# Performance work log

Hardware: AMD Instinct MI355X
Metric: run time of the kernel (lower is better)

## Reference

```python
import jax, jax.numpy as jnp
import numpy as np

NC = 120000            # active coarse voxels
D, H, W = 16, 256, 256 # coarse grid
NF = 2 * NC            # active fine voxels (upsample output)
CIN, COUT = 128, 64


def _build_pairs():
    """Build spconv-style (in_idx, out_idx) pair maps per kernel offset.
    Padding: in_idx = NC (dummy zero feature row), out_idx = n_out (dropped row)."""
    rng = np.random.default_rng(0)
    flat = rng.choice(D * H * W, size=NC, replace=False)
    cz, cy, cx = np.unravel_index(flat, (D, H, W))
    lut = np.full(D * H * W, -1, np.int64)
    lut[flat] = np.arange(NC)

    def subm(offs):
        P = np.full((len(offs), NC, 2), NC, np.int32)
        for k, (dz, dy, dx) in enumerate(offs):
            nz, ny, nx = cz + dz, cy + dy, cx + dx
            ok = (nz >= 0) & (nz < D) & (ny >= 0) & (ny < H) & (nx >= 0) & (nx < W)
            nb = np.full(NC, -1, np.int64)
            nb[ok] = lut[(nz[ok] * H + ny[ok]) * W + nx[ok]]
            ok &= nb >= 0
            idx = np.nonzero(ok)[0]
            P[k, :len(idx), 0] = nb[idx]
            P[k, :len(idx), 1] = idx
        return P

    o33 = [(a, b, c) for a in (-1, 0, 1) for b in (-1, 0, 1) for c in (-1, 0, 1)]
    o13 = [(0, b, c) for b in (-1, 0, 1) for c in (-1, 0, 1)]   # kernel (1,3,3)
    o31 = [(a, 0, c) for a in (-1, 0, 1) for c in (-1, 0, 1)]   # kernel (3,1,3)

    # fine coords: each coarse voxel c spawns fine voxels 2c and 2c+1 (all dims)
    fz = np.concatenate([cz * 2, cz * 2 + 1])
    fy = np.concatenate([cy * 2, cy * 2 + 1])
    fx = np.concatenate([cx * 2, cx * 2 + 1])
    # inverse of a k=3, stride=2, pad=1 downsample: fine f <- coarse o where f = 2o - 1 + k
    Pu = np.zeros((27, NC, 2), np.int32)
    Pu[..., 0] = NC
    Pu[..., 1] = NF
    for k, (a, b, c) in enumerate([(a, b, c) for a in range(3) for b in range(3) for c in range(3)]):
        nz, ny, nx = fz + 1 - a, fy + 1 - b, fx + 1 - c
        ok = (nz % 2 == 0) & (ny % 2 == 0) & (nx % 2 == 0) & (nz >= 0) & (ny >= 0) & (nx >= 0)
        oz, oy, ox = nz // 2, ny // 2, nx // 2
        ok &= (oz < D) & (oy < H) & (ox < W)
        nb = np.full(NF, -1, np.int64)
        nb[ok] = lut[(oz[ok] * H + oy[ok]) * W + ox[ok]]
        ok &= nb >= 0
        idx = np.nonzero(ok)[0][:NC]
        Pu[k, :len(idx), 0] = nb[idx]
        Pu[k, :len(idx), 1] = idx
    return subm(o33), subm(o13), subm(o31), Pu


def setup_inputs():
    p33, p13, p31, pup = _build_pairs()
    ks = jax.random.split(jax.random.key(0), 12)
    f32 = jnp.float32
    return {
        "feats_x": jax.random.normal(ks[0], (NC, CIN), f32),
        "feats_skip": jax.random.normal(ks[1], (NC, CIN), f32),
        "W_trans": 0.05 * jax.random.normal(ks[2], (27, CIN, COUT), f32),
        "W1": 0.05 * jax.random.normal(ks[3], (9, COUT, COUT), f32),
        "W2": 0.05 * jax.random.normal(ks[4], (9, COUT, COUT), f32),
        "W_up": 0.05 * jax.random.normal(ks[5], (27, COUT, COUT), f32),
        "g0": 1.0 + 0.1 * jax.random.normal(ks[6], (COUT,), f32),
        "b0": 0.1 * jax.random.normal(ks[7], (COUT,), f32),
        "g1": 1.0 + 0.1 * jax.random.normal(ks[8], (COUT,), f32),
        "b1": 0.1 * jax.random.normal(ks[9], (COUT,), f32),
        "g2": 1.0 + 0.1 * jax.random.normal(ks[10], (COUT,), f32),
        "b2": 0.1 * jax.random.normal(ks[11], (COUT,), f32),
        "pairs33": jnp.asarray(p33),
        "pairs13": jnp.asarray(p13),
        "pairs31": jnp.asarray(p31),
        "pairs_up": jnp.asarray(pup),
    }


def _spconv(feats, Wk, pairs, n_out):
    # gather-GEMM-scatter sparse conv: feats [N,Cin], Wk [K,Cin,Cout], pairs [K,P,2]
    fp = jnp.concatenate([feats, jnp.zeros((1, feats.shape[1]), feats.dtype)], 0)
    out = jnp.zeros((n_out + 1, Wk.shape[2]), feats.dtype)
    for k in range(Wk.shape[0]):  # fixed small K (9 or 27)
        msg = fp[pairs[k, :, 0]] @ Wk[k]        # [P, Cout]
        out = out.at[pairs[k, :, 1]].add(msg)
    return out[:n_out]


def _bn(x, g, b):
    # BatchNorm1d (training-mode batch stats, eps=1e-5, biased var)
    m = x.mean(0)
    v = x.var(0)
    return (x - m) * jax.lax.rsqrt(v + 1e-5) * g + b


def reference(feats_x, feats_skip, W_trans, W1, W2, W_up,
              g0, b0, g1, b1, g2, b2,
              pairs33, pairs13, pairs31, pairs_up):
    x = feats_x + feats_skip                              # residual fuse with skip
    upA = _spconv(x, W_trans, pairs33, NC)                # trans_dilao (3x3x3 subm)
    upA = _bn(jax.nn.leaky_relu(upA, 0.01), g0, b0)       # act then BN (as in source)
    upE1 = _bn(_spconv(upA, W1, pairs13, NC), g1, b1)     # conv1x3 + bn1
    upE2 = _bn(_spconv(upA, W2, pairs31, NC), g2, b2)     # conv3x1 + bn2
    return _spconv(upE1 + upE2, W_up, pairs_up, NF)       # SparseInverseConv3d upsample
```

## Files before the change

kernel.cpp:

```cpp
#include <hip/hip_runtime.h>
#include <stdint.h>

typedef unsigned short u16;
typedef unsigned int u32;
typedef __bf16 bf16x8 __attribute__((ext_vector_type(8)));
typedef float floatx4 __attribute__((ext_vector_type(4)));

static constexpr int NC = 120000;
static constexpr int NF = 240000;

__device__ __forceinline__ float bf2f(u16 u) {
    union { u32 i; float f; } v; v.i = ((u32)u) << 16; return v.f;
}
__device__ __forceinline__ u16 f2bf(float f) {
    union { float f; u32 i; } v; v.f = f;
    u32 r = v.i + 0x7FFFu + ((v.i >> 16) & 1u);
    return (u16)(r >> 16);
}

__global__ void add_pad_k(const float* __restrict__ a, const float* __restrict__ b,
                          u16* __restrict__ xp) {
    int idx = blockIdx.x * blockDim.x + threadIdx.x;
    if (idx >= (NC + 1) * 32) return;
    uint2 vo;
    if (idx < NC * 32) {
        float4 va = ((const float4*)a)[idx];
        float4 vb = ((const float4*)b)[idx];
        vo.x = (u32)f2bf(va.x + vb.x) | ((u32)f2bf(va.y + vb.y) << 16);
        vo.y = (u32)f2bf(va.z + vb.z) | ((u32)f2bf(va.w + vb.w) << 16);
    } else {
        vo.x = vo.y = 0u;
    }
    ((uint2*)xp)[idx] = vo;
}

__global__ void transpose_w_k(const float* __restrict__ W, u16* __restrict__ Wt,
                              int K, int Cin) {
    int idx = blockIdx.x * blockDim.x + threadIdx.x;
    if (idx >= K * Cin * 64) return;
    int per = Cin * 64;
    int k = idx / per, rem = idx - k * per;
    int kc = rem >> 11;
    int r2 = rem & 2047;
    int nt = r2 >> 9, lane = (r2 >> 3) & 63, j = r2 & 7;
    int ci = kc * 32 + (lane >> 4) * 8 + j;
    int co = nt * 16 + (lane & 15);
    Wt[idx] = f2bf(W[(size_t)(k * Cin + ci) * 64 + co]);
}

__device__ __forceinline__ int upslot_to_k(int s) {
    if (s == 4) return 13;
    int e = s < 4 ? s : s - 5;
    int base = s < 4 ? 0 : 18;
    return base + 2 * e + ((e >> 1) << 1);
}
__global__ void transpose_wup_k(const float* __restrict__ W, u16* __restrict__ Wt) {
    int idx = blockIdx.x * blockDim.x + threadIdx.x;
    if (idx >= 9 * 4096) return;
    int s = idx >> 12, rem = idx & 4095;
    int kc = rem >> 11, r2 = rem & 2047;
    int nt = r2 >> 9, lane = (r2 >> 3) & 63, j = r2 & 7;
    int ci = kc * 32 + (lane >> 4) * 8 + j;
    int co = nt * 16 + (lane & 15);
    int k = upslot_to_k(s);
    Wt[idx] = f2bf(W[(size_t)(k * 64 + ci) * 64 + co]);
}

__global__ void fill_k(int* __restrict__ p, int n, int val) {
    int i = blockIdx.x * blockDim.x + threadIdx.x;
    if (i < n) p[i] = val;
}

__global__ void scatter_k(const int* __restrict__ pairs, int* __restrict__ inv,
                          int npairs, int n_out) {
    int i = blockIdx.x * blockDim.x + threadIdx.x;
    if (i >= npairs) return;
    int in = pairs[2 * i], out = pairs[2 * i + 1];
    if (out < n_out) inv[(i / NC) * n_out + out] = in;
}

__global__ void scatter_up_k(const int* __restrict__ pairs, int* __restrict__ inv) {
    int i = blockIdx.x * blockDim.x + threadIdx.x;
    if (i >= 27 * NC) return;
    int in = pairs[2 * i], out = pairs[2 * i + 1];
    if (out >= NF) return;
    int k = i / NC;
    int a = k / 9, r = k - a * 9, b = r / 3, c = r - b * 3;
    int s;
    if (k == 13) {
        s = 4;
    } else if (((a | b | c) & 1) == 0) {
        int e = (a >> 1) * 4 + (b >> 1) * 2 + (c >> 1);
        s = e < 4 ? e : e + 1;
    } else {
        return;
    }
    inv[(size_t)s * NF + out] = in;
}

template <int TCIN, int K, int R, bool LEAKY, bool F32OUT, int MINW>
__global__ __launch_bounds__(256, MINW) void spconv_k(
    const u16* __restrict__ feats,
    const int* __restrict__ invA, const u16* __restrict__ wTA, void* __restrict__ outA,
    const int* __restrict__ invB, const u16* __restrict__ wTB, void* __restrict__ outB,
    int nb0, int n_outA, int n_outB) {
    constexpr int KC = TCIN / 32;
    const int tid = threadIdx.x;
    const int wave = tid >> 6, lane = tid & 63;
    const int l15 = lane & 15, quad = lane >> 4;
    const bool second = (int)blockIdx.x >= nb0;
    const int bid = second ? (int)blockIdx.x - nb0 : (int)blockIdx.x;
    const int* __restrict__ inv = second ? invB : invA;
    const u16* __restrict__ wT  = second ? wTB : wTA;
    void* __restrict__ outv     = second ? outB : outA;
    const int n_out             = second ? n_outB : n_outA;

    const int blockrow = bid * (R * 64);
    const int base = blockrow + wave * 16 + l15;

    floatx4 acc[R][4];
#pragma unroll
    for (int t = 0; t < R; ++t)
#pragma unroll
        for (int nt = 0; nt < 4; ++nt) acc[t][nt] = (floatx4)(0.0f);

    int rc[R], rn[R];
#pragma unroll
    for (int t = 0; t < R; ++t) rc[t] = inv[base + t * 64];
#pragma unroll
    for (int t = 0; t < R; ++t) rn[t] = inv[n_out + base + t * 64];

    bf16x8 abuf[2][R][KC];
#pragma unroll
    for (int t = 0; t < R; ++t) {
        if (__any(rc[t] != NC)) {
            const u16* ap = feats + (size_t)rc[t] * TCIN + quad * 8;
#pragma unroll
            for (int kc = 0; kc < KC; ++kc) abuf[0][t][kc] = *(const bf16x8*)(ap + kc * 32);
        }
    }

#pragma unroll
    for (int k = 0; k < K; ++k) {
        const int cur = k & 1, nxt = cur ^ 1;
        int rf[R];
#pragma unroll
        for (int t = 0; t < R; ++t) rf[t] = NC;
        if (k + 2 < K) {
            const int* invf = inv + (size_t)(k + 2) * n_out;
#pragma unroll
            for (int t = 0; t < R; ++t) rf[t] = invf[base + t * 64];
        }
        bool lv[R], any = false;
#pragma unroll
        for (int t = 0; t < R; ++t) { lv[t] = __any(rc[t] != NC); any = any || lv[t]; }
        bf16x8 b[KC][4];
        if (any) {
            const u16* wk = wT + (size_t)k * (64 * TCIN);
#pragma unroll
            for (int kc = 0; kc < KC; ++kc)
#pragma unroll
                for (int nt = 0; nt < 4; ++nt)
                    b[kc][nt] = *(const bf16x8*)(wk + ((kc * 4 + nt) * 64 + lane) * 8);
        }
        if (k + 1 < K) {
#pragma unroll
            for (int t = 0; t < R; ++t) {
                if (__any(rn[t] != NC)) {
                    const u16* ap = feats + (size_t)rn[t] * TCIN + quad * 8;
#pragma unroll
                    for (int kc = 0; kc < KC; ++kc) abuf[nxt][t][kc] = *(const bf16x8*)(ap + kc * 32);
                }
            }
        }
#pragma unroll
        for (int t = 0; t < R; ++t) {
            if (lv[t]) {
#pragma unroll
                for (int kc = 0; kc < KC; ++kc)
#pragma unroll
                    for (int nt = 0; nt < 4; ++nt)
                        acc[t][nt] = __builtin_amdgcn_mfma_f32_16x16x32_bf16(
                            abuf[cur][t][kc], b[kc][nt], acc[t][nt], 0, 0, 0);
            }
        }
#pragma unroll
        for (int t = 0; t < R; ++t) { rc[t] = rn[t]; rn[t] = rf[t]; }
    }
#pragma unroll
    for (int t = 0; t < R; ++t) {
#pragma unroll
        for (int nt = 0; nt < 4; ++nt) {
#pragma unroll
            for (int r = 0; r < 4; ++r) {
                float v = acc[t][nt][r];
                if (LEAKY) v = v > 0.f ? v : 0.01f * v;
                int row = blockrow + t * 64 + wave * 16 + quad * 4 + r;
                size_t oi = (size_t)row * 64 + nt * 16 + l15;
                if (F32OUT) ((float*)outv)[oi] = v;
                else        ((u16*)outv)[oi] = f2bf(v);
            }
        }
    }
}

__global__ void stats2_k(const u16* __restrict__ ra, const u16* __restrict__ rb,
                         float* __restrict__ sa, float* __restrict__ sb, int half) {
    const u16* raw = ((int)blockIdx.x < half) ? ra : rb;
    float* sums    = ((int)blockIdx.x < half) ? sa : sb;
    int bx = ((int)blockIdx.x < half) ? (int)blockIdx.x : (int)blockIdx.x - half;
    int tid = threadIdx.x;
    int wave = tid >> 6, c = tid & 63;
    int gw = bx * 4 + wave;
    int GW = half * 4;
    float s = 0.f, q = 0.f;
    for (int r = gw; r < NC; r += GW) {
        float v = bf2f(raw[(size_t)r * 64 + c]);
        s += v; q += v * v;
    }
    __shared__ float sbm[4][64], qbm[4][64];
    sbm[wave][c] = s; qbm[wave][c] = q;
    __syncthreads();
    if (tid < 64) {
        float S = sbm[0][tid] + sbm[1][tid] + sbm[2][tid] + sbm[3][tid];
        float Q = qbm[0][tid] + qbm[1][tid] + qbm[2][tid] + qbm[3][tid];
        atomicAdd(&sums[tid], S);
        atomicAdd(&sums[64 + tid], Q);
    }
}

template <bool F32IN>
__global__ void stats_pair_k(const void* __restrict__ ra, const void* __restrict__ rb,
                             float* __restrict__ sums, int nblk) {
    int tid = threadIdx.x;
    int wave = tid >> 6, c = tid & 63;
    int gw = (int)blockIdx.x * 4 + wave;
    int GW = nblk * 4;
    float s = 0.f, q = 0.f;
    for (int r = gw; r < NC; r += GW) {
        size_t o = (size_t)r * 64 + c;
        float v = F32IN ? (((const float*)ra)[o] + ((const float*)rb)[o])
                        : (bf2f(((const u16*)ra)[o]) + bf2f(((const u16*)rb)[o]));
        v = v > 0.f ? v : 0.01f * v;
        s += v; q += v * v;
    }
    __shared__ float sbm[4][64], qbm[4][64];
    sbm[wave][c] = s; qbm[wave][c] = q;
    __syncthreads();
    if (tid < 64) {
        float S = sbm[0][tid] + sbm[1][tid] + sbm[2][tid] + sbm[3][tid];
        float Q = qbm[0][tid] + qbm[1][tid] + qbm[2][tid] + qbm[3][tid];
        atomicAdd(&sums[tid], S);
        atomicAdd(&sums[64 + tid], Q);
    }
}

__global__ void finalize_k(const float* __restrict__ sums, const float* __restrict__ g,
                           const float* __restrict__ bb, float* __restrict__ scsh) {
    int c = threadIdx.x;
    if (c < 64) {
        float m = sums[c] / (float)NC;
        float v = sums[64 + c] / (float)NC - m * m;
        float sc = g[c] * rsqrtf(v + 1e-5f);
        scsh[c] = sc;
        scsh[64 + c] = bb[c] - m * sc;
    }
}

template <bool F32IN>
__global__ void apply_pair_k(const void* __restrict__ ra, const void* __restrict__ rb,
                             const float* __restrict__ scsh, u16* __restrict__ up) {
    int idx = blockIdx.x * blockDim.x + threadIdx.x;
    if (idx >= (NC + 1) * 64) return;
    int c = idx & 63, i = idx >> 6;
    u16 o = 0;
    if (i < NC) {
        float v = F32IN ? (((const float*)ra)[idx] + ((const float*)rb)[idx])
                        : (bf2f(((const u16*)ra)[idx]) + bf2f(((const u16*)rb)[idx]));
        v = v > 0.f ? v : 0.01f * v;
        o = f2bf(v * scsh[c] + scsh[64 + c]);
    }
    up[idx] = o;
}

__global__ void apply12_k(const u16* __restrict__ rb, const u16* __restrict__ rc,
                          const float* __restrict__ s1, const float* __restrict__ s2,
                          u16* __restrict__ up) {
    int idx = blockIdx.x * blockDim.x + threadIdx.x;
    if (idx >= (NC + 1) * 64) return;
    int c = idx & 63, i = idx >> 6;
    float v = bf2f(rb[idx]) * s1[c] + s1[64 + c] + bf2f(rc[idx]) * s2[c] + s2[64 + c];
    up[idx] = (i < NC) ? f2bf(v) : (u16)0;
}

extern "C" void kernel_launch(void* const* d_in, const int* in_sizes, int n_in,
                              void* d_out, int out_size, void* d_ws, size_t ws_size,
                              hipStream_t stream) {
    const float* feats_x    = (const float*)d_in[0];
    const float* feats_skip = (const float*)d_in[1];
    const float* W_trans    = (const float*)d_in[2];
    const float* W1         = (const float*)d_in[3];
    const float* W2         = (const float*)d_in[4];
    const float* W_up       = (const float*)d_in[5];
    const float* g0 = (const float*)d_in[6],  *b0 = (const float*)d_in[7];
    const float* g1 = (const float*)d_in[8],  *b1 = (const float*)d_in[9];
    const float* g2 = (const float*)d_in[10], *b2 = (const float*)d_in[11];
    const int* pairs33 = (const int*)d_in[12];
    const int* pairs13 = (const int*)d_in[13];
    const int* pairs31 = (const int*)d_in[14];
    const int* pairs_up = (const int*)d_in[15];
    float* outp = (float*)d_out;

    const bool bigws = ws_size >= (size_t)130267392;

    char* ws = (char*)d_ws;
    size_t off = 0;
    auto alloc = [&](size_t bytes) {
        char* p = ws + off;
        off += (bytes + 255) & ~(size_t)255;
        return p;
    };
    u16* xp    = (u16*)alloc(30720256);
    int* inv33 = (int*)alloc(13440000);
    int* inv13 = (int*)alloc(4320000);
    int* inv31 = (int*)alloc(4320000);
    void* rawF0 = (void*)alloc(bigws ? 30720000 : 15360000);
    void* rawF1 = (void*)alloc(bigws ? 30720000 : 15360000);
    u16* upA   = (u16*)alloc(15360128);
    u16* WtA   = (u16*)alloc(27 * 128 * 64 * 2);
    u16* Wt1   = (u16*)alloc(9 * 64 * 64 * 2);
    u16* Wt2   = (u16*)alloc(9 * 64 * 64 * 2);
    u16* WtU   = (u16*)alloc(9 * 64 * 64 * 2);
    float* stats = (float*)alloc(6 * 128 * 4);
    int* inv_up = (int*)xp;
    u16* rawB = (u16*)rawF0;
    u16* rawC = (u16*)rawF1;
    u16* upE  = (u16*)inv33;
    float *sums0 = stats,        *sums1 = stats + 128, *sums2 = stats + 256;
    float *scsh0 = stats + 384,  *scsh1 = stats + 512, *scsh2 = stats + 640;

    const int B = 256;
    hipMemsetAsync(stats, 0, 6 * 128 * 4, stream);

    transpose_w_k<<<(27 * 128 * 64 + 255) / 256, B, 0, stream>>>(W_trans, WtA, 27, 128);
    transpose_w_k<<<(9 * 64 * 64 + 255) / 256, B, 0, stream>>>(W1, Wt1, 9, 64);
    transpose_w_k<<<(9 * 64 * 64 + 255) / 256, B, 0, stream>>>(W2, Wt2, 9, 64);
    transpose_wup_k<<<(9 * 64 * 64 + 255) / 256, B, 0, stream>>>(W_up, WtU);

    add_pad_k<<<((NC + 1) * 32 + 255) / 256, B, 0, stream>>>(feats_x, feats_skip, xp);

    fill_k<<<(46 * NC + 255) / 256, B, 0, stream>>>(inv33, 46 * NC, NC);
    scatter_k<<<(27 * NC + 255) / 256, B, 0, stream>>>(pairs33, inv33, 27 * NC, NC);
    scatter_k<<<(9 * NC + 255) / 256, B, 0, stream>>>(pairs13, inv13, 9 * NC, NC);
    scatter_k<<<(9 * NC + 255) / 256, B, 0, stream>>>(pairs31, inv31, 9 * NC, NC);

    if (bigws) {
        spconv_k<128, 14, 3, false, true, 2><<<1250, B, 0, stream>>>(
            xp, inv33, WtA, rawF0, inv33 + 14 * NC, WtA + 14 * 128 * 64, rawF1,
            625, NC, NC);
        stats_pair_k<true><<<240, B, 0, stream>>>(rawF0, rawF1, sums0, 240);
        finalize_k<<<1, 64, 0, stream>>>(sums0, g0, b0, scsh0);
        apply_pair_k<true><<<((NC + 1) * 64 + 255) / 256, B, 0, stream>>>(
            rawF0, rawF1, scsh0, upA);
    } else {
        spconv_k<128, 14, 3, false, false, 2><<<1250, B, 0, stream>>>(
            xp, inv33, WtA, rawF0, inv33 + 14 * NC, WtA + 14 * 128 * 64, rawF1,
            625, NC, NC);
        stats_pair_k<false><<<240, B, 0, stream>>>(rawF0, rawF1, sums0, 240);
        finalize_k<<<1, 64, 0, stream>>>(sums0, g0, b0, scsh0);
        apply_pair_k<false><<<((NC + 1) * 64 + 255) / 256, B, 0, stream>>>(
            rawF0, rawF1, scsh0, upA);
    }

    fill_k<<<(9 * NF + 255) / 256, B, 0, stream>>>(inv_up, 9 * NF, NC);
    scatter_up_k<<<(27 * NC + 255) / 256, B, 0, stream>>>(pairs_up, inv_up);

    spconv_k<64, 9, 3, false, false, 3><<<1250, B, 0, stream>>>(
        upA, inv13, Wt1, rawB, inv31, Wt2, rawC, 625, NC, NC);
    stats2_k<<<240, B, 0, stream>>>(rawB, rawC, sums1, sums2, 120);
    finalize_k<<<1, 64, 0, stream>>>(sums1, g1, b1, scsh1);
    finalize_k<<<1, 64, 0, stream>>>(sums2, g2, b2, scsh2);

    apply12_k<<<((NC + 1) * 64 + 255) / 256, B, 0, stream>>>(rawB, rawC, scsh1, scsh2, upE);

    spconv_k<64, 9, 3, false, true, 3><<<1250, B, 0, stream>>>(
        upE, inv_up, WtU, outp, inv_up, WtU, outp, 1250, NF, NF);
}
```

Measured before the change: 540.7 us.

## Stage weights through LDS and skip provably empty upsample kernel offsets

Each block now copies its per-offset weight slice from global memory into a double-buffered LDS array and reads it from there, with a block barrier after every offset. The first conv uses a runtime live-offset count (14 and 13) instead of running a padded 28th slice, so the inv33 buffer shrinks by one slice. The upsample slots are reordered so the centre offset comes first. The upsample conv is then split: rows below NC run only the centre offset, and rows at or above NC run only the eight corner offsets. This removes weight fetches that every wave repeated and skips offsets known to have no pairs, at the cost of extra barriers and LDS use that may lower occupancy.

```diff
diff --git a/kernel.cpp b/kernel.cpp
--- a/kernel.cpp
+++ b/kernel.cpp
@@ -49,10 +49,9 @@
 }
 
 __device__ __forceinline__ int upslot_to_k(int s) {
-    if (s == 4) return 13;
-    int e = s < 4 ? s : s - 5;
-    int base = s < 4 ? 0 : 18;
-    return base + 2 * e + ((e >> 1) << 1);
+    if (s == 0) return 13;
+    int e = s - 1;
+    return 18 * ((e >> 2) & 1) + 6 * ((e >> 1) & 1) + 2 * (e & 1);
 }
 __global__ void transpose_wup_k(const float* __restrict__ W, u16* __restrict__ Wt) {
     int idx = blockIdx.x * blockDim.x + threadIdx.x;
@@ -88,23 +87,26 @@
     int a = k / 9, r = k - a * 9, b = r / 3, c = r - b * 3;
     int s;
     if (k == 13) {
-        s = 4;
+        s = 0;
     } else if (((a | b | c) & 1) == 0) {
-        int e = (a >> 1) * 4 + (b >> 1) * 2 + (c >> 1);
-        s = e < 4 ? e : e + 1;
+        s = 1 + (a >> 1) * 4 + (b >> 1) * 2 + (c >> 1);
     } else {
         return;
     }
     inv[(size_t)s * NF + out] = in;
 }
 
-template <int TCIN, int K, int R, bool LEAKY, bool F32OUT, int MINW>
+template <int TCIN, int KMAX, int R, bool F32OUT, int MINW>
 __global__ __launch_bounds__(256, MINW) void spconv_k(
     const u16* __restrict__ feats,
     const int* __restrict__ invA, const u16* __restrict__ wTA, void* __restrict__ outA,
     const int* __restrict__ invB, const u16* __restrict__ wTB, void* __restrict__ outB,
-    int nb0, int n_outA, int n_outB) {
+    int nb0, int n_outA, int n_outB, int kliveA, int kliveB) {
     constexpr int KC = TCIN / 32;
+    constexpr int WFRAGS = TCIN * 64 / 8;
+    constexpr int NST = WFRAGS / 256;
+    __shared__ bf16x8 wlds[2][WFRAGS];
+
     const int tid = threadIdx.x;
     const int wave = tid >> 6, lane = tid & 63;
     const int l15 = lane & 15, quad = lane >> 4;
@@ -114,6 +116,7 @@
     const u16* __restrict__ wT  = second ? wTB : wTA;
     void* __restrict__ outv     = second ? outB : outA;
     const int n_out             = second ? n_outB : n_outA;
+    const int Klive             = second ? kliveB : kliveA;
 
     const int blockrow = bid * (R * 64);
     const int base = blockrow + wave * 16 + l15;
@@ -129,6 +132,12 @@
     for (int t = 0; t < R; ++t) rc[t] = inv[base + t * 64];
 #pragma unroll
     for (int t = 0; t < R; ++t) rn[t] = inv[n_out + base + t * 64];
+
+    {
+        const bf16x8* wsrc = (const bf16x8*)wT + tid;
+#pragma unroll
+        for (int s = 0; s < NST; ++s) wlds[0][tid + s * 256] = wsrc[s * 256];
+    }
 
     bf16x8 abuf[2][R][KC];
 #pragma unroll
@@ -139,53 +148,65 @@
             for (int kc = 0; kc < KC; ++kc) abuf[0][t][kc] = *(const bf16x8*)(ap + kc * 32);
         }
     }
-
-#pragma unroll
-    for (int k = 0; k < K; ++k) {
-        const int cur = k & 1, nxt = cur ^ 1;
-        int rf[R];
-#pragma unroll
-        for (int t = 0; t < R; ++t) rf[t] = NC;
-        if (k + 2 < K) {
-            const int* invf = inv + (size_t)(k + 2) * n_out;
-#pragma unroll
-            for (int t = 0; t < R; ++t) rf[t] = invf[base + t * 64];
-        }
-        bool lv[R], any = false;
-#pragma unroll
-        for (int t = 0; t < R; ++t) { lv[t] = __any(rc[t] != NC); any = any || lv[t]; }
-        bf16x8 b[KC][4];
-        if (any) {
-            const u16* wk = wT + (size_t)k * (64 * TCIN);
-#pragma unroll
-            for (int kc = 0; kc < KC; ++kc)
-#pragma unroll
-                for (int nt = 0; nt < 4; ++nt)
-                    b[kc][nt] = *(const bf16x8*)(wk + ((kc * 4 + nt) * 64 + lane) * 8);
-        }
-        if (k + 1 < K) {
-#pragma unroll
-            for (int t = 0; t < R; ++t) {
-                if (__any(rn[t] != NC)) {
-                    const u16* ap = feats + (size_t)rn[t] * TCIN + quad * 8;
-#pragma unroll
-                    for (int kc = 0; kc < KC; ++kc) abuf[nxt][t][kc] = *(const bf16x8*)(ap + kc * 32);
+    __syncthreads();
+
+#pragma unroll
+    for (int k = 0; k < KMAX; ++k) {
+        if (k < Klive) {
+            const int cur = k & 1, nxt = cur ^ 1;
+            if (k + 1 < Klive) {
+                const bf16x8* wsrc = (const bf16x8*)(wT + (size_t)(k + 1) * (64 * TCIN)) + tid;
+                bf16x8 st[NST];
+#pragma unroll
+                for (int s = 0; s < NST; ++s) st[s] = wsrc[s * 256];
+#pragma unroll
+                for (int s = 0; s < NST; ++s) wlds[nxt][tid + s * 256] = st[s];
+            }
+            int rf[R];
+#pragma unroll
+            for (int t = 0; t < R; ++t) rf[t] = NC;
+            if (k + 2 < Klive) {
+                const int* invf = inv + (size_t)(k + 2) * n_out;
+#pragma unroll
+                for (int t = 0; t < R; ++t) rf[t] = invf[base + t * 64];
+            }
+            bool lv[R], any = false;
+#pragma unroll
+            for (int t = 0; t < R; ++t) { lv[t] = __any(rc[t] != NC); any = any || lv[t]; }
+            if (k + 1 < Klive) {
+#pragma unroll
+                for (int t = 0; t < R; ++t) {
+                    if (__any(rn[t] != NC)) {
+                        const u16* ap = feats + (size_t)rn[t] * TCIN + quad * 8;
+#pragma unroll
+                        for (int kc = 0; kc < KC; ++kc)
+                            abuf[nxt][t][kc] = *(const bf16x8*)(ap + kc * 32);
+                    }
                 }
             }
+            if (any) {
+                bf16x8 b[KC][4];
+#pragma unroll
+                for (int kc = 0; kc < KC; ++kc)
+#pragma unroll
+                    for (int nt = 0; nt < 4; ++nt)
+                        b[kc][nt] = wlds[cur][(kc * 4 + nt) * 64 + lane];
+#pragma unroll
+                for (int t = 0; t < R; ++t) {
+                    if (lv[t]) {
+#pragma unroll
+                        for (int kc = 0; kc < KC; ++kc)
+#pragma unroll
+                            for (int nt = 0; nt < 4; ++nt)
+                                acc[t][nt] = __builtin_amdgcn_mfma_f32_16x16x32_bf16(
+                                    abuf[cur][t][kc], b[kc][nt], acc[t][nt], 0, 0, 0);
+                    }
+                }
+            }
+            __syncthreads();
+#pragma unroll
+            for (int t = 0; t < R; ++t) { rc[t] = rn[t]; rn[t] = rf[t]; }
         }
-#pragma unroll
-        for (int t = 0; t < R; ++t) {
-            if (lv[t]) {
-#pragma unroll
-                for (int kc = 0; kc < KC; ++kc)
-#pragma unroll
-                    for (int nt = 0; nt < 4; ++nt)
-                        acc[t][nt] = __builtin_amdgcn_mfma_f32_16x16x32_bf16(
-                            abuf[cur][t][kc], b[kc][nt], acc[t][nt], 0, 0, 0);
-            }
-        }
-#pragma unroll
-        for (int t = 0; t < R; ++t) { rc[t] = rn[t]; rn[t] = rf[t]; }
     }
 #pragma unroll
     for (int t = 0; t < R; ++t) {
@@ -194,7 +215,6 @@
 #pragma unroll
             for (int r = 0; r < 4; ++r) {
                 float v = acc[t][nt][r];
-                if (LEAKY) v = v > 0.f ? v : 0.01f * v;
                 int row = blockrow + t * 64 + wave * 16 + quad * 4 + r;
                 size_t oi = (size_t)row * 64 + nt * 16 + l15;
                 if (F32OUT) ((float*)outv)[oi] = v;
@@ -321,7 +341,7 @@
         return p;
     };
     u16* xp    = (u16*)alloc(30720256);
-    int* inv33 = (int*)alloc(13440000);
+    int* inv33 = (int*)alloc(12960000);
     int* inv13 = (int*)alloc(4320000);
     int* inv31 = (int*)alloc(4320000);
     void* rawF0 = (void*)alloc(bigws ? 30720000 : 15360000);
@@ -349,23 +369,23 @@
 
     add_pad_k<<<((NC + 1) * 32 + 255) / 256, B, 0, stream>>>(feats_x, feats_skip, xp);
 
-    fill_k<<<(46 * NC + 255) / 256, B, 0, stream>>>(inv33, 46 * NC, NC);
+    fill_k<<<(45 * NC + 255) / 256, B, 0, stream>>>(inv33, 45 * NC, NC);
     scatter_k<<<(27 * NC + 255) / 256, B, 0, stream>>>(pairs33, inv33, 27 * NC, NC);
     scatter_k<<<(9 * NC + 255) / 256, B, 0, stream>>>(pairs13, inv13, 9 * NC, NC);
     scatter_k<<<(9 * NC + 255) / 256, B, 0, stream>>>(pairs31, inv31, 9 * NC, NC);
 
     if (bigws) {
-        spconv_k<128, 14, 3, false, true, 2><<<1250, B, 0, stream>>>(
+        spconv_k<128, 14, 3, true, 2><<<1250, B, 0, stream>>>(
             xp, inv33, WtA, rawF0, inv33 + 14 * NC, WtA + 14 * 128 * 64, rawF1,
-            625, NC, NC);
+            625, NC, NC, 14, 13);
         stats_pair_k<true><<<240, B, 0, stream>>>(rawF0, rawF1, sums0, 240);
         finalize_k<<<1, 64, 0, stream>>>(sums0, g0, b0, scsh0);
         apply_pair_k<true><<<((NC + 1) * 64 + 255) / 256, B, 0, stream>>>(
             rawF0, rawF1, scsh0, upA);
     } else {
-        spconv_k<128, 14, 3, false, false, 2><<<1250, B, 0, stream>>>(
+        spconv_k<128, 14, 3, false, 2><<<1250, B, 0, stream>>>(
             xp, inv33, WtA, rawF0, inv33 + 14 * NC, WtA + 14 * 128 * 64, rawF1,
-            625, NC, NC);
+            625, NC, NC, 14, 13);
         stats_pair_k<false><<<240, B, 0, stream>>>(rawF0, rawF1, sums0, 240);
         finalize_k<<<1, 64, 0, stream>>>(sums0, g0, b0, scsh0);
         apply_pair_k<false><<<((NC + 1) * 64 + 255) / 256, B, 0, stream>>>(
@@ -375,14 +395,16 @@
     fill_k<<<(9 * NF + 255) / 256, B, 0, stream>>>(inv_up, 9 * NF, NC);
     scatter_up_k<<<(27 * NC + 255) / 256, B, 0, stream>>>(pairs_up, inv_up);
 
-    spconv_k<64, 9, 3, false, false, 3><<<1250, B, 0, stream>>>(
-        upA, inv13, Wt1, rawB, inv31, Wt2, rawC, 625, NC, NC);
+    spconv_k<64, 9, 3, false, 3><<<1250, B, 0, stream>>>(
+        upA, inv13, Wt1, rawB, inv31, Wt2, rawC, 625, NC, NC, 9, 9);
     stats2_k<<<240, B, 0, stream>>>(rawB, rawC, sums1, sums2, 120);
     finalize_k<<<1, 64, 0, stream>>>(sums1, g1, b1, scsh1);
     finalize_k<<<1, 64, 0, stream>>>(sums2, g2, b2, scsh2);
 
     apply12_k<<<((NC + 1) * 64 + 255) / 256, B, 0, stream>>>(rawB, rawC, scsh1, scsh2, upE);
 
-    spconv_k<64, 9, 3, false, true, 3><<<1250, B, 0, stream>>>(
-        upE, inv_up, WtU, outp, inv_up, WtU, outp, 1250, NF, NF);
-}
+    spconv_k<64, 8, 3, true, 3><<<1250, B, 0, stream>>>(
+        upE, inv_up, WtU, outp,
+        inv_up + (size_t)NF + NC, WtU + 64 * 64, (void*)(outp + (size_t)NC * 64),
+        625, NF, NF, 1, 8);
+}
```

Result: no change. 533.3 us (-1.4%).

## Replace gather-based inverse maps with dense center tap plus atomic scatter over compacted pairs

Applied to the files above, without the earlier changes.

Drops the fill/scatter inverse-map construction. The identity centre tap of each convolution, and the two identity-like upsample taps, are now computed as dense GEMMs that write fp32 outputs directly. The remaining taps are processed over the valid prefix of each pair list, found by binary search, using weights staged in LDS and fp32 atomicAdd scatter. This removes the work wasted on padded rows and the inverse-map traffic, at the cost of atomic contention and fp32 intermediates.

```diff
diff --git a/kernel.cpp b/kernel.cpp
--- a/kernel.cpp
+++ b/kernel.cpp
@@ -49,10 +49,9 @@
 }
 
 __device__ __forceinline__ int upslot_to_k(int s) {
-    if (s == 4) return 13;
-    int e = s < 4 ? s : s - 5;
-    int base = s < 4 ? 0 : 18;
-    return base + 2 * e + ((e >> 1) << 1);
+    if (s == 0) return 13;
+    int e = s - 1;
+    return 18 * ((e >> 2) & 1) + 6 * ((e >> 1) & 1) + 2 * (e & 1);
 }
 __global__ void transpose_wup_k(const float* __restrict__ W, u16* __restrict__ Wt) {
     int idx = blockIdx.x * blockDim.x + threadIdx.x;
@@ -66,156 +65,212 @@
     Wt[idx] = f2bf(W[(size_t)(k * 64 + ci) * 64 + co]);
 }
 
-__global__ void fill_k(int* __restrict__ p, int n, int val) {
-    int i = blockIdx.x * blockDim.x + threadIdx.x;
-    if (i < n) p[i] = val;
-}
-
-__global__ void scatter_k(const int* __restrict__ pairs, int* __restrict__ inv,
-                          int npairs, int n_out) {
-    int i = blockIdx.x * blockDim.x + threadIdx.x;
-    if (i >= npairs) return;
-    int in = pairs[2 * i], out = pairs[2 * i + 1];
-    if (out < n_out) inv[(i / NC) * n_out + out] = in;
-}
-
-__global__ void scatter_up_k(const int* __restrict__ pairs, int* __restrict__ inv) {
-    int i = blockIdx.x * blockDim.x + threadIdx.x;
-    if (i >= 27 * NC) return;
-    int in = pairs[2 * i], out = pairs[2 * i + 1];
-    if (out >= NF) return;
-    int k = i / NC;
-    int a = k / 9, r = k - a * 9, b = r / 3, c = r - b * 3;
-    int s;
-    if (k == 13) {
-        s = 4;
-    } else if (((a | b | c) & 1) == 0) {
-        int e = (a >> 1) * 4 + (b >> 1) * 2 + (c >> 1);
-        s = e < 4 ? e : e + 1;
-    } else {
-        return;
-    }
-    inv[(size_t)s * NF + out] = in;
-}
-
-template <int TCIN, int K, int R, bool LEAKY, bool F32OUT, int MINW>
-__global__ __launch_bounds__(256, MINW) void spconv_k(
-    const u16* __restrict__ feats,
-    const int* __restrict__ invA, const u16* __restrict__ wTA, void* __restrict__ outA,
-    const int* __restrict__ invB, const u16* __restrict__ wTB, void* __restrict__ outB,
-    int nb0, int n_outA, int n_outB) {
+__global__ void counts_k(const int* __restrict__ p33, const int* __restrict__ p13,
+                         const int* __restrict__ p31, const int* __restrict__ pup,
+                         int* __restrict__ meta) {
+    __shared__ int cl[64];
+    const int t = threadIdx.x;
+    const int* pp = nullptr;
+    int n_out = NC;
+    if (t < 26) {
+        int k = t + (t >= 13);
+        pp = p33 + (size_t)k * 2 * NC;
+    } else if (t >= 32 && t < 48) {
+        int j = t - 32, w = j >> 3, jj = j & 7, k = jj + (jj >= 4);
+        pp = (w ? p31 : p13) + (size_t)k * 2 * NC;
+    } else if (t >= 56 && t < 63) {
+        const int kup[7] = {0, 2, 6, 8, 18, 20, 24};
+        pp = pup + (size_t)kup[t - 56] * 2 * NC;
+        n_out = NF;
+    }
+    if (pp) {
+        int lo = 0, hi = NC;
+        while (lo < hi) {
+            int mid = (lo + hi) >> 1;
+            if (pp[2 * mid + 1] < n_out) lo = mid + 1; else hi = mid;
+        }
+        cl[t] = lo;
+    }
+    __syncthreads();
+    if (t == 0) {
+        int acc = 0;
+        for (int i = 0; i < 26; ++i) {
+            meta[1 + i] = acc; meta[1 + 26 + i] = cl[i];
+            acc += (cl[i] + 255) >> 8;
+        }
+        meta[0] = acc;
+    }
+    if (t == 1) {
+        int acc = 0;
+        for (int i = 0; i < 16; ++i) {
+            meta[65 + i] = acc; meta[65 + 16 + i] = cl[32 + i];
+            acc += (cl[32 + i] + 255) >> 8;
+        }
+        meta[64] = acc;
+    }
+    if (t == 2) {
+        int acc = 0;
+        for (int i = 0; i < 7; ++i) {
+            meta[129 + i] = acc; meta[129 + 7 + i] = cl[56 + i];
+            acc += (cl[56 + i] + 255) >> 8;
+        }
+        meta[128] = acc;
+    }
+}
+
+template <int TCIN, bool DUAL>
+__global__ __launch_bounds__(256, 2) void dense_k(
+    const u16* __restrict__ feats, const u16* __restrict__ W0,
+    const u16* __restrict__ W1, float* __restrict__ out0,
+    float* __restrict__ out1, int nrows) {
     constexpr int KC = TCIN / 32;
     const int tid = threadIdx.x;
     const int wave = tid >> 6, lane = tid & 63;
     const int l15 = lane & 15, quad = lane >> 4;
-    const bool second = (int)blockIdx.x >= nb0;
-    const int bid = second ? (int)blockIdx.x - nb0 : (int)blockIdx.x;
-    const int* __restrict__ inv = second ? invB : invA;
-    const u16* __restrict__ wT  = second ? wTB : wTA;
-    void* __restrict__ outv     = second ? outB : outA;
-    const int n_out             = second ? n_outB : n_outA;
-
-    const int blockrow = bid * (R * 64);
-    const int base = blockrow + wave * 16 + l15;
-
-    floatx4 acc[R][4];
-#pragma unroll
-    for (int t = 0; t < R; ++t)
-#pragma unroll
-        for (int nt = 0; nt < 4; ++nt) acc[t][nt] = (floatx4)(0.0f);
-
-    int rc[R], rn[R];
-#pragma unroll
-    for (int t = 0; t < R; ++t) rc[t] = inv[base + t * 64];
-#pragma unroll
-    for (int t = 0; t < R; ++t) rn[t] = inv[n_out + base + t * 64];
-
-    bf16x8 abuf[2][R][KC];
-#pragma unroll
-    for (int t = 0; t < R; ++t) {
-        if (__any(rc[t] != NC)) {
-            const u16* ap = feats + (size_t)rc[t] * TCIN + quad * 8;
-#pragma unroll
-            for (int kc = 0; kc < KC; ++kc) abuf[0][t][kc] = *(const bf16x8*)(ap + kc * 32);
-        }
-    }
-
-#pragma unroll
-    for (int k = 0; k < K; ++k) {
-        const int cur = k & 1, nxt = cur ^ 1;
-        int rf[R];
-#pragma unroll
-        for (int t = 0; t < R; ++t) rf[t] = NC;
-        if (k + 2 < K) {
-            const int* invf = inv + (size_t)(k + 2) * n_out;
-#pragma unroll
-            for (int t = 0; t < R; ++t) rf[t] = invf[base + t * 64];
-        }
-        bool lv[R], any = false;
-#pragma unroll
-        for (int t = 0; t < R; ++t) { lv[t] = __any(rc[t] != NC); any = any || lv[t]; }
-        bf16x8 b[KC][4];
-        if (any) {
-            const u16* wk = wT + (size_t)k * (64 * TCIN);
-#pragma unroll
-            for (int kc = 0; kc < KC; ++kc)
-#pragma unroll
-                for (int nt = 0; nt < 4; ++nt)
-                    b[kc][nt] = *(const bf16x8*)(wk + ((kc * 4 + nt) * 64 + lane) * 8);
-        }
-        if (k + 1 < K) {
-#pragma unroll
-            for (int t = 0; t < R; ++t) {
-                if (__any(rn[t] != NC)) {
-                    const u16* ap = feats + (size_t)rn[t] * TCIN + quad * 8;
-#pragma unroll
-                    for (int kc = 0; kc < KC; ++kc) abuf[nxt][t][kc] = *(const bf16x8*)(ap + kc * 32);
+    bf16x8 b0[KC][4], b1[DUAL ? KC : 1][4];
+#pragma unroll
+    for (int kc = 0; kc < KC; ++kc)
+#pragma unroll
+        for (int nt = 0; nt < 4; ++nt) {
+            b0[kc][nt] = *(const bf16x8*)(W0 + ((kc * 4 + nt) * 64 + lane) * 8);
+            if (DUAL) b1[kc][nt] = *(const bf16x8*)(W1 + ((kc * 4 + nt) * 64 + lane) * 8);
+        }
+#pragma unroll
+    for (int i = 0; i < 2; ++i) {
+        const int row0 = (int)blockIdx.x * 128 + wave * 32 + i * 16;
+        int r = row0 + l15;
+        const u16* ap = feats + (size_t)min(r, nrows) * TCIN + quad * 8;
+        bf16x8 a[KC];
+#pragma unroll
+        for (int kc = 0; kc < KC; ++kc) a[kc] = *(const bf16x8*)(ap + kc * 32);
+        floatx4 ac0[4], ac1[4];
+#pragma unroll
+        for (int nt = 0; nt < 4; ++nt) { ac0[nt] = (floatx4)(0.0f); ac1[nt] = (floatx4)(0.0f); }
+#pragma unroll
+        for (int kc = 0; kc < KC; ++kc)
+#pragma unroll
+            for (int nt = 0; nt < 4; ++nt) {
+                ac0[nt] = __builtin_amdgcn_mfma_f32_16x16x32_bf16(a[kc], b0[kc][nt], ac0[nt], 0, 0, 0);
+                if (DUAL)
+                    ac1[nt] = __builtin_amdgcn_mfma_f32_16x16x32_bf16(a[kc], b1[kc][nt], ac1[nt], 0, 0, 0);
+            }
+#pragma unroll
+        for (int nt = 0; nt < 4; ++nt)
+#pragma unroll
+            for (int rr = 0; rr < 4; ++rr) {
+                int orow = row0 + quad * 4 + rr;
+                if (orow < nrows) {
+                    size_t oi = (size_t)orow * 64 + nt * 16 + l15;
+                    out0[oi] = ac0[nt][rr];
+                    if (DUAL) out1[oi] = ac1[nt][rr];
                 }
             }
-        }
-#pragma unroll
-        for (int t = 0; t < R; ++t) {
-            if (lv[t]) {
+    }
+}
+
+template <int TCIN, int MODE, int T>
+__global__ __launch_bounds__(256, 2) void sparse_k(
+    const u16* __restrict__ feats,
+    const int* __restrict__ P0, const int* __restrict__ P1,
+    const u16* __restrict__ W0, const u16* __restrict__ W1,
+    float* __restrict__ out0, float* __restrict__ out1,
+    const int* __restrict__ meta, int n_out) {
+    constexpr int KC = TCIN / 32;
+    constexpr int NW = TCIN * 64 / 8;
+    constexpr int NST = NW / 256;
+    __shared__ bf16x8 wlds[NW];
+    const int tid = threadIdx.x;
+    const int wave = tid >> 6, lane = tid & 63;
+    const int l15 = lane & 15, quad = lane >> 4;
+    const int total = meta[0];
+    for (int item = (int)blockIdx.x; item < total; item += (int)gridDim.x) {
+        int t = 0;
+#pragma unroll
+        for (int i = 1; i < T; ++i) t += (item >= meta[1 + i]);
+        const int cnt = meta[1 + T + t];
+        const int* pp;
+        const u16* wt;
+        float* op;
+        if (MODE == 0) {
+            int k = t + (t >= 13);
+            pp = P0 + (size_t)k * 2 * NC;
+            wt = W0 + (size_t)k * TCIN * 64;
+            op = out0;
+        } else if (MODE == 1) {
+            int j = t & 7, k = j + (j >= 4);
+            pp = (t >= 8 ? P1 : P0) + (size_t)k * 2 * NC;
+            wt = (t >= 8 ? W1 : W0) + (size_t)k * TCIN * 64;
+            op = t >= 8 ? out1 : out0;
+        } else {
+            const int kup[7] = {0, 2, 6, 8, 18, 20, 24};
+            pp = P0 + (size_t)kup[t] * 2 * NC;
+            wt = W0 + (size_t)(t + 1) * TCIN * 64;
+            op = out0;
+        }
+        __syncthreads();
+#pragma unroll
+        for (int s = 0; s < NST; ++s) wlds[tid + s * 256] = ((const bf16x8*)wt)[tid + s * 256];
+        __syncthreads();
+        const int pbase = (item - meta[1 + t]) * 256 + wave * 64;
+        bf16x8 abuf[2][KC];
+        {
+            int p = pbase + l15;
+            int in = (p >= cnt) ? NC : P0[0];
+            in = (p >= cnt) ? NC : pp[2 * min(p, NC - 1)];
+            const u16* ap = feats + (size_t)in * TCIN + quad * 8;
+#pragma unroll
+            for (int kc = 0; kc < KC; ++kc) abuf[0][kc] = *(const bf16x8*)(ap + kc * 32);
+        }
+#pragma unroll
+        for (int i = 0; i < 4; ++i) {
+            const int cur = i & 1, nxt = cur ^ 1;
+            const int tb = pbase + i * 16;
+            if (i + 1 < 4) {
+                int p = tb + 16 + l15;
+                int in = (p >= cnt) ? NC : pp[2 * min(p, NC - 1)];
+                const u16* ap = feats + (size_t)in * TCIN + quad * 8;
+#pragma unroll
+                for (int kc = 0; kc < KC; ++kc) abuf[nxt][kc] = *(const bf16x8*)(ap + kc * 32);
+            }
+            if (tb < cnt) {
+                floatx4 acc[4];
+#pragma unroll
+                for (int nt = 0; nt < 4; ++nt) acc[nt] = (floatx4)(0.0f);
 #pragma unroll
                 for (int kc = 0; kc < KC; ++kc)
 #pragma unroll
                     for (int nt = 0; nt < 4; ++nt)
-                        acc[t][nt] = __builtin_amdgcn_mfma_f32_16x16x32_bf16(
-                            abuf[cur][t][kc], b[kc][nt], acc[t][nt], 0, 0, 0);
+                        acc[nt] = __builtin_amdgcn_mfma_f32_16x16x32_bf16(
+                            abuf[cur][kc], wlds[(kc * 4 + nt) * 64 + lane], acc[nt], 0, 0, 0);
+#pragma unroll
+                for (int r = 0; r < 4; ++r) {
+                    int pr = tb + quad * 4 + r;
+                    if (pr < cnt) {
+                        int o = pp[2 * min(pr, NC - 1) + 1];
+                        if (o < n_out) {
+                            size_t ob = (size_t)o * 64 + l15;
+#pragma unroll
+                            for (int nt = 0; nt < 4; ++nt)
+                                atomicAdd(&op[ob + nt * 16], acc[nt][r]);
+                        }
+                    }
+                }
             }
         }
-#pragma unroll
-        for (int t = 0; t < R; ++t) { rc[t] = rn[t]; rn[t] = rf[t]; }
-    }
-#pragma unroll
-    for (int t = 0; t < R; ++t) {
-#pragma unroll
-        for (int nt = 0; nt < 4; ++nt) {
-#pragma unroll
-            for (int r = 0; r < 4; ++r) {
-                float v = acc[t][nt][r];
-                if (LEAKY) v = v > 0.f ? v : 0.01f * v;
-                int row = blockrow + t * 64 + wave * 16 + quad * 4 + r;
-                size_t oi = (size_t)row * 64 + nt * 16 + l15;
-                if (F32OUT) ((float*)outv)[oi] = v;
-                else        ((u16*)outv)[oi] = f2bf(v);
-            }
-        }
-    }
-}
-
-__global__ void stats2_k(const u16* __restrict__ ra, const u16* __restrict__ rb,
-                         float* __restrict__ sa, float* __restrict__ sb, int half) {
-    const u16* raw = ((int)blockIdx.x < half) ? ra : rb;
-    float* sums    = ((int)blockIdx.x < half) ? sa : sb;
-    int bx = ((int)blockIdx.x < half) ? (int)blockIdx.x : (int)blockIdx.x - half;
+    }
+}
+
+template <bool LEAKY>
+__global__ void stats_f32_k(const float* __restrict__ raw, float* __restrict__ sums,
+                            int nblk) {
     int tid = threadIdx.x;
     int wave = tid >> 6, c = tid & 63;
-    int gw = bx * 4 + wave;
-    int GW = half * 4;
+    int gw = (int)blockIdx.x * 4 + wave;
+    int GW = nblk * 4;
     float s = 0.f, q = 0.f;
     for (int r = gw; r < NC; r += GW) {
-        float v = bf2f(raw[(size_t)r * 64 + c]);
+        float v = raw[(size_t)r * 64 + c];
+        if (LEAKY) v = v > 0.f ? v : 0.01f * v;
         s += v; q += v * v;
     }
     __shared__ float sbm[4][64], qbm[4][64];
@@ -229,19 +284,18 @@
     }
 }
 
-template <bool F32IN>
-__global__ void stats_pair_k(const void* __restrict__ ra, const void* __restrict__ rb,
-                             float* __restrict__ sums, int nblk) {
+__global__ void stats2f_k(const float* __restrict__ ra, const float* __restrict__ rb,
+                          float* __restrict__ sa, float* __restrict__ sb, int half) {
+    const float* raw = ((int)blockIdx.x < half) ? ra : rb;
+    float* sums      = ((int)blockIdx.x < half) ? sa : sb;
+    int bx = ((int)blockIdx.x < half) ? (int)blockIdx.x : (int)blockIdx.x - half;
     int tid = threadIdx.x;
     int wave = tid >> 6, c = tid & 63;
-    int gw = (int)blockIdx.x * 4 + wave;
-    int GW = nblk * 4;
+    int gw = bx * 4 + wave;
+    int GW = half * 4;
     float s = 0.f, q = 0.f;
     for (int r = gw; r < NC; r += GW) {
-        size_t o = (size_t)r * 64 + c;
-        float v = F32IN ? (((const float*)ra)[o] + ((const float*)rb)[o])
-                        : (bf2f(((const u16*)ra)[o]) + bf2f(((const u16*)rb)[o]));
-        v = v > 0.f ? v : 0.01f * v;
+        float v = raw[(size_t)r * 64 + c];
         s += v; q += v * v;
     }
     __shared__ float sbm[4][64], qbm[4][64];
@@ -267,30 +321,33 @@
     }
 }
 
-template <bool F32IN>
-__global__ void apply_pair_k(const void* __restrict__ ra, const void* __restrict__ rb,
-                             const float* __restrict__ scsh, u16* __restrict__ up) {
+template <bool LEAKY>
+__global__ void apply_f32_k(const float* __restrict__ raw, const float* __restrict__ scsh,
+                            u16* __restrict__ up) {
     int idx = blockIdx.x * blockDim.x + threadIdx.x;
     if (idx >= (NC + 1) * 64) return;
     int c = idx & 63, i = idx >> 6;
     u16 o = 0;
     if (i < NC) {
-        float v = F32IN ? (((const float*)ra)[idx] + ((const float*)rb)[idx])
-                        : (bf2f(((const u16*)ra)[idx]) + bf2f(((const u16*)rb)[idx]));
-        v = v > 0.f ? v : 0.01f * v;
+        float v = raw[idx];
+        if (LEAKY) v = v > 0.f ? v : 0.01f * v;
         o = f2bf(v * scsh[c] + scsh[64 + c]);
     }
     up[idx] = o;
 }
 
-__global__ void apply12_k(const u16* __restrict__ rb, const u16* __restrict__ rc,
-                          const float* __restrict__ s1, const float* __restrict__ s2,
-                          u16* __restrict__ up) {
+__global__ void apply12f_k(const float* __restrict__ rb, const float* __restrict__ rc,
+                           const float* __restrict__ s1, const float* __restrict__ s2,
+                           u16* __restrict__ up) {
     int idx = blockIdx.x * blockDim.x + threadIdx.x;
     if (idx >= (NC + 1) * 64) return;
     int c = idx & 63, i = idx >> 6;
-    float v = bf2f(rb[idx]) * s1[c] + s1[64 + c] + bf2f(rc[idx]) * s2[c] + s2[64 + c];
-    up[idx] = (i < NC) ? f2bf(v) : (u16)0;
+    u16 o = 0;
+    if (i < NC) {
+        float v = rb[idx] * s1[c] + s1[64 + c] + rc[idx] * s2[c] + s2[64 + c];
+        o = f2bf(v);
+    }
+    up[idx] = o;
 }
 
 extern "C" void kernel_launch(void* const* d_in, const int* in_sizes, int n_in,
@@ -311,8 +368,6 @@
     const int* pairs_up = (const int*)d_in[15];
     float* outp = (float*)d_out;
 
-    const bool bigws = ws_size >= (size_t)130267392;
-
     char* ws = (char*)d_ws;
     size_t off = 0;
     auto alloc = [&](size_t bytes) {
@@ -320,22 +375,18 @@
         off += (bytes + 255) & ~(size_t)255;
         return p;
     };
-    u16* xp    = (u16*)alloc(30720256);
-    int* inv33 = (int*)alloc(13440000);
-    int* inv13 = (int*)alloc(4320000);
-    int* inv31 = (int*)alloc(4320000);
-    void* rawF0 = (void*)alloc(bigws ? 30720000 : 15360000);
-    void* rawF1 = (void*)alloc(bigws ? 30720000 : 15360000);
-    u16* upA   = (u16*)alloc(15360128);
+    u16* xp       = (u16*)alloc(30720256);
+    float* rawA32 = (float*)alloc(30720000);
+    float* rawC32 = (float*)alloc(30720000);
     u16* WtA   = (u16*)alloc(27 * 128 * 64 * 2);
     u16* Wt1   = (u16*)alloc(9 * 64 * 64 * 2);
     u16* Wt2   = (u16*)alloc(9 * 64 * 64 * 2);
     u16* WtU   = (u16*)alloc(9 * 64 * 64 * 2);
     float* stats = (float*)alloc(6 * 128 * 4);
-    int* inv_up = (int*)xp;
-    u16* rawB = (u16*)rawF0;
-    u16* rawC = (u16*)rawF1;
-    u16* upE  = (u16*)inv33;
+    int* meta  = (int*)alloc(1024);
+    u16* upA = xp;
+    u16* upE = (u16*)((char*)xp + 15360128);
+    float* rawB32 = rawA32;
     float *sums0 = stats,        *sums1 = stats + 128, *sums2 = stats + 256;
     float *scsh0 = stats + 384,  *scsh1 = stats + 512, *scsh2 = stats + 640;
 
@@ -348,41 +399,27 @@
     transpose_wup_k<<<(9 * 64 * 64 + 255) / 256, B, 0, stream>>>(W_up, WtU);
 
     add_pad_k<<<((NC + 1) * 32 + 255) / 256, B, 0, stream>>>(feats_x, feats_skip, xp);
-
-    fill_k<<<(46 * NC + 255) / 256, B, 0, stream>>>(inv33, 46 * NC, NC);
-    scatter_k<<<(27 * NC + 255) / 256, B, 0, stream>>>(pairs33, inv33, 27 * NC, NC);
-    scatter_k<<<(9 * NC + 255) / 256, B, 0, stream>>>(pairs13, inv13, 9 * NC, NC);
-    scatter_k<<<(9 * NC + 255) / 256, B, 0, stream>>>(pairs31, inv31, 9 * NC, NC);
-
-    if (bigws) {
-        spconv_k<128, 14, 3, false, true, 2><<<1250, B, 0, stream>>>(
-            xp, inv33, WtA, rawF0, inv33 + 14 * NC, WtA + 14 * 128 * 64, rawF1,
-            625, NC, NC);
-        stats_pair_k<true><<<240, B, 0, stream>>>(rawF0, rawF1, sums0, 240);
-        finalize_k<<<1, 64, 0, stream>>>(sums0, g0, b0, scsh0);
-        apply_pair_k<true><<<((NC + 1) * 64 + 255) / 256, B, 0, stream>>>(
-            rawF0, rawF1, scsh0, upA);
-    } else {
-        spconv_k<128, 14, 3, false, false, 2><<<1250, B, 0, stream>>>(
-            xp, inv33, WtA, rawF0, inv33 + 14 * NC, WtA + 14 * 128 * 64, rawF1,
-            625, NC, NC);
-        stats_pair_k<false><<<240, B, 0, stream>>>(rawF0, rawF1, sums0, 240);
-        finalize_k<<<1, 64, 0, stream>>>(sums0, g0, b0, scsh0);
-        apply_pair_k<false><<<((NC + 1) * 64 + 255) / 256, B, 0, stream>>>(
-            rawF0, rawF1, scsh0, upA);
-    }
-
-    fill_k<<<(9 * NF + 255) / 256, B, 0, stream>>>(inv_up, 9 * NF, NC);
-    scatter_up_k<<<(27 * NC + 255) / 256, B, 0, stream>>>(pairs_up, inv_up);
-
-    spconv_k<64, 9, 3, false, false, 3><<<1250, B, 0, stream>>>(
-        upA, inv13, Wt1, rawB, inv31, Wt2, rawC, 625, NC, NC);
-    stats2_k<<<240, B, 0, stream>>>(rawB, rawC, sums1, sums2, 120);
+    counts_k<<<1, 64, 0, stream>>>(pairs33, pairs13, pairs31, pairs_up, meta);
+
+    dense_k<128, false><<<938, B, 0, stream>>>(
+        xp, WtA + 13 * 128 * 64, WtA, rawA32, rawA32, NC);
+    sparse_k<128, 0, 26><<<2048, B, 0, stream>>>(
+        xp, pairs33, pairs33, WtA, WtA, rawA32, rawA32, meta, NC);
+    stats_f32_k<true><<<240, B, 0, stream>>>(rawA32, sums0, 240);
+    finalize_k<<<1, 64, 0, stream>>>(sums0, g0, b0, scsh0);
+    apply_f32_k<true><<<((NC + 1) * 64 + 255) / 256, B, 0, stream>>>(rawA32, scsh0, upA);
+
+    dense_k<64, true><<<938, B, 0, stream>>>(
+        upA, Wt1 + 4 * 64 * 64, Wt2 + 4 * 64 * 64, rawB32, rawC32, NC);
+    sparse_k<64, 1, 16><<<1024, B, 0, stream>>>(
+        upA, pairs13, pairs31, Wt1, Wt2, rawB32, rawC32, meta + 64, NC);
+    stats2f_k<<<240, B, 0, stream>>>(rawB32, rawC32, sums1, sums2, 120);
     finalize_k<<<1, 64, 0, stream>>>(sums1, g1, b1, scsh1);
     finalize_k<<<1, 64, 0, stream>>>(sums2, g2, b2, scsh2);
-
-    apply12_k<<<((NC + 1) * 64 + 255) / 256, B, 0, stream>>>(rawB, rawC, scsh1, scsh2, upE);
-
-    spconv_k<64, 9, 3, false, true, 3><<<1250, B, 0, stream>>>(
-        upE, inv_up, WtU, outp, inv_up, WtU, outp, 1250, NF, NF);
-}
+    apply12f_k<<<((NC + 1) * 64 + 255) / 256, B, 0, stream>>>(rawB32, rawC32, scsh1, scsh2, upE);
+
+    dense_k<64, true><<<938, B, 0, stream>>>(
+        upE, WtU, WtU + 8 * 64 * 64, outp, outp + (size_t)NC * 64, NC);
+    sparse_k<64, 2, 7><<<512, B, 0, stream>>>(
+        upE, pairs_up, pairs_up, WtU, WtU, outp, outp, meta + 128, NF);
+}
```

After: 549.1 us. About the same (+1.6%).
